# Performance work log

Measured on AMD Instinct MI355X. Metric: run time of the kernel, lower is better.

Reference implementation:

```python
import jax, jax.numpy as jnp
import numpy as np

N = 100000   # product nodes
E = 300000   # edges per relation
DIN = 128    # node_feature_dim
H = 128      # hidden_dim
NEG_SLOPE = 0.2


def setup_inputs() -> dict:
    key = jax.random.key(0)
    ks = iter(jax.random.split(key, 64))
    def nrm(shape, scale):
        return (jax.random.normal(next(ks), shape) * scale).astype(jnp.float32)
    d = {}
    d["x"] = nrm((N, DIN), 1.0)
    d["pos"] = nrm((N, 3), 1.0)
    for name in ("ei_chem", "ei_cond", "ei_mol"):
        d[name] = jax.random.randint(next(ks), (2, E), 0, N, dtype=jnp.int32)
    s = 1.0 / np.sqrt(H)
    d["Wp"] = nrm((DIN, H), 1.0 / np.sqrt(DIN)); d["bp"] = jnp.zeros((H,), jnp.float32)
    for L in ("1", "2"):
        for r in ("c", "d"):  # chemical_transformation, condition_modulation: heads=2
            d[f"W{L}{r}"] = nrm((H, H), s)
            d[f"as{L}{r}"] = nrm((2, H // 2), s)
            d[f"ad{L}{r}"] = nrm((2, H // 2), s)
            d[f"b{L}{r}"] = jnp.zeros((H,), jnp.float32)
        # molecule_target (EQGAT): heads=4
        d[f"W{L}m"] = nrm((H, H), s)
        d[f"as{L}m"] = nrm((4, H // 4), s)
        d[f"ad{L}m"] = nrm((4, H // 4), s)
        d[f"b{L}m"] = jnp.zeros((H,), jnp.float32)
        d[f"Wl{L}"] = nrm((H, H), s)
        d[f"bl{L}"] = jnp.zeros((H,), jnp.float32)
    d["Wy"] = nrm((H, 1), s); d["by"] = jnp.zeros((1,), jnp.float32)
    d["Wa"] = nrm((H, 1), s); d["ba"] = jnp.zeros((1,), jnp.float32)
    return d


def gat_conv(x, row, col, W, a_s, a_d, bias, heads, n):
    """PyG-style GATConv (concat=True, add_self_loops=True)."""
    Fh = W.shape[1] // heads
    loops = jnp.arange(n, dtype=row.dtype)
    row = jnp.concatenate([row, loops])
    col = jnp.concatenate([col, loops])
    h = (x @ W).reshape(n, heads, Fh)                      # [n,Hd,Fh]
    alpha_s = jnp.einsum('nhf,hf->nh', h, a_s)             # [n,Hd]
    alpha_d = jnp.einsum('nhf,hf->nh', h, a_d)
    e = jax.nn.leaky_relu(alpha_s[row] + alpha_d[col], NEG_SLOPE)  # [E',Hd]
    m = jax.lax.stop_gradient(jax.ops.segment_max(e, col, num_segments=n))
    ex = jnp.exp(e - m[col])
    z = jax.ops.segment_sum(ex, col, num_segments=n)
    alpha = ex / (z[col] + 1e-16)                          # per-dst softmax
    msg = h[row] * alpha[:, :, None]                       # [E',Hd,Fh]
    out = jax.ops.segment_sum(msg, col, num_segments=n).reshape(n, heads * Fh)
    return out + bias


def eqgat(x, pos, row, col, W, a_s, a_d, bias, Wl, bl, heads, n):
    geo = jnp.sqrt(jnp.sum((pos[row] - pos[col]) ** 2, axis=-1))  # [E]
    x = x + 0.1 * geo.mean()                                       # scalar broadcast
    h = gat_conv(x, row, col, W, a_s, a_d, bias, heads, n)
    return h @ Wl + bl


def reference(x, pos, ei_chem, ei_cond, ei_mol,
              Wp, bp,
              W1c, as1c, ad1c, b1c, W1d, as1d, ad1d, b1d,
              W1m, as1m, ad1m, b1m, Wl1, bl1,
              W2c, as2c, ad2c, b2c, W2d, as2d, ad2d, b2d,
              W2m, as2m, ad2m, b2m, Wl2, bl2,
              Wy, by, Wa, ba):
    n = x.shape[0]
    h0 = x @ Wp + bp
    h1 = jax.nn.relu(
        gat_conv(h0, ei_chem[0], ei_chem[1], W1c, as1c, ad1c, b1c, 2, n)
        + gat_conv(h0, ei_cond[0], ei_cond[1], W1d, as1d, ad1d, b1d, 2, n)
        + eqgat(h0, pos, ei_mol[0], ei_mol[1], W1m, as1m, ad1m, b1m, Wl1, bl1, 4, n))
    h2 = jax.nn.relu(
        gat_conv(h1, ei_chem[0], ei_chem[1], W2c, as2c, ad2c, b2c, 2, n)
        + gat_conv(h1, ei_cond[0], ei_cond[1], W2d, as2d, ad2d, b2d, 2, n)
        + eqgat(h1, pos, ei_mol[0], ei_mol[1], W2m, as2m, ad2m, b2m, Wl2, bl2, 4, n))
    pred_yield = (h2 @ Wy + by).squeeze(-1)
    pred_activity = (h2 @ Wa + ba).squeeze(-1)
    return jnp.stack([pred_yield, pred_activity], axis=-1)  # [n,2]
```

## Files before the change

kernel.cpp:

```cpp
#include <hip/hip_runtime.h>
#include <math.h>

typedef short short8 __attribute__((ext_vector_type(8)));
typedef float f32x4 __attribute__((ext_vector_type(4)));
typedef unsigned short us4 __attribute__((ext_vector_type(4)));

#define MAXDEG 32
#define GF_BIAS   1
#define GF_CSHIFT 2
#define GF_ALPHA  4
#define NFRAG 18432

__device__ __forceinline__ unsigned short f2bf(float f) {
  unsigned u = __float_as_uint(f);
  u += 0x7FFF + ((u >> 16) & 1);
  return (unsigned short)(u >> 16);
}
__device__ __forceinline__ float bf2f(unsigned short s) { return __uint_as_float(((unsigned)s) << 16); }
__device__ __forceinline__ float lrelu(float v) { return v > 0.f ? v : 0.2f * v; }

__global__ __launch_bounds__(256) void k_scatter3(
    const int* __restrict__ ei0, const int* __restrict__ ei1, const int* __restrict__ ei2,
    int* __restrict__ cur,
    int* __restrict__ s0, int* __restrict__ s1, int* __restrict__ s2,
    const float* __restrict__ pos, float* __restrict__ gsum, int E, int N) {
  __shared__ float part[4];
  const int t = blockIdx.x * 256 + threadIdx.x;
  float d = 0.f;
  if (t < 3 * E) {
    int rel, e;
    if (t < E)          { rel = 0; e = t; }
    else if (t < 2 * E) { rel = 1; e = t - E; }
    else                { rel = 2; e = t - 2 * E; }
    const int* ei = (rel == 0) ? ei0 : (rel == 1) ? ei1 : ei2;
    int* srcs     = (rel == 0) ? s0  : (rel == 1) ? s1  : s2;
    const int r = ei[e];
    const int c = ei[E + e];
    const int slot = atomicAdd(&cur[rel * N + c], 1);
    if (slot < MAXDEG) srcs[(size_t)c * MAXDEG + slot] = r;
    if (rel == 2) {
      const float dx = pos[3*r]   - pos[3*c];
      const float dy = pos[3*r+1] - pos[3*c+1];
      const float dz = pos[3*r+2] - pos[3*c+2];
      d = sqrtf(dx*dx + dy*dy + dz*dz);
    }
  }
  #pragma unroll
  for (int o = 32; o; o >>= 1) d += __shfl_down(d, o);
  if ((threadIdx.x & 63) == 0) part[threadIdx.x >> 6] = d;
  __syncthreads();
  if (threadIdx.x == 0) {
    const float s = part[0] + part[1] + part[2] + part[3];
    if (s != 0.f) atomicAdd(gsum, s);
  }
}

struct PrepArgs {
  const float* W[9];
  const float* as_[9];
  const float* ad_[9];
  unsigned short* hi[9];
  unsigned short* lo[9];
  float* csum[9];
  int fh[9];
};

__global__ __launch_bounds__(256) void k_prep(PrepArgs p) {
  const int s = blockIdx.x;
  const int t = threadIdx.x;
  const float* W = p.W[s];
  const int fh = p.fh[s];
  __shared__ float Ws[128 * 129];
  __shared__ float alpha[128 * 8];
  {
    const f32x4* src = (const f32x4*)W;
    for (int i = t; i < 4096; i += 256) {
      const f32x4 v = src[i];
      const int row = i >> 5;
      const int col = (i & 31) * 4;
      float* dst = &Ws[row * 129 + col];
      dst[0] = v[0]; dst[1] = v[1]; dst[2] = v[2]; dst[3] = v[3];
    }
  }
  __syncthreads();
  if (t < 128) {
    #pragma unroll
    for (int a = 0; a < 8; ++a) alpha[t * 8 + a] = 0.f;
    if (fh) {
      const int nh = 128 / fh;
      for (int h = 0; h < nh; ++h) {
        float s1 = 0.f, s2 = 0.f;
        for (int c = 0; c < fh; ++c) {
          const float w = Ws[t * 129 + h * fh + c];
          s1 += w * p.as_[s][h * fh + c];
          s2 += w * p.ad_[s][h * fh + c];
        }
        alpha[t * 8 + h] = s1;
        alpha[t * 8 + 4 + h] = s2;
      }
    }
  }
  __syncthreads();
  for (int idx = t; idx < NFRAG; idx += 256) {
    const int j = idx & 7, lane = (idx >> 3) & 63, kt = (idx >> 9) & 3, nt = idx >> 11;
    const int k = kt * 32 + (lane >> 4) * 8 + j;
    const int col = nt * 16 + (lane & 15);
    float w;
    if (col < 128) w = Ws[k * 129 + col];
    else if (col < 136) w = alpha[k * 8 + (col - 128)];
    else w = 0.f;
    const unsigned short h = f2bf(w);
    p.hi[s][idx] = h;
    p.lo[s][idx] = f2bf(w - bf2f(h));
  }
  if (t < 136) {
    float cs = 0.f;
    if (t < 128) for (int k = 0; k < 128; ++k) cs += Ws[k * 129 + t];
    else         for (int k = 0; k < 128; ++k) cs += alpha[k * 8 + (t - 128)];
    p.csum[s][t] = cs;
  }
}

__global__ __launch_bounds__(256, 2) void k_gmm(
    const float* __restrict__ A, const unsigned short* __restrict__ Whi,
    const unsigned short* __restrict__ Wlo, const float* __restrict__ csum,
    const float* __restrict__ bias, unsigned short* __restrict__ C,
    float* __restrict__ aS, float* __restrict__ aD,
    const float* __restrict__ gsum, float gscale,
    int n, int npad, int flags)
{
  __shared__ unsigned short shi[NFRAG];
  __shared__ unsigned short slo[NFRAG];
  {
    const f32x4* srch = (const f32x4*)Whi;
    const f32x4* srcl = (const f32x4*)Wlo;
    f32x4* dsth = (f32x4*)shi;
    f32x4* dstl = (f32x4*)slo;
    for (int i = threadIdx.x; i < NFRAG / 8; i += 256) { dsth[i] = srch[i]; dstl[i] = srcl[i]; }
  }
  __syncthreads();

  const int wave = threadIdx.x >> 6, lane = threadIdx.x & 63;
  const int m = lane & 15, kq = lane >> 4;
  const float cb = (flags & GF_CSHIFT) ? gscale * gsum[0] : 0.f;

  for (int rb = blockIdx.x * 128; rb < npad; rb += gridDim.x * 128) {
    const int rw = rb + wave * 32;
    short8 ah[2][4], al[2][4];
    #pragma unroll
    for (int sub = 0; sub < 2; ++sub) {
      const int row = rw + sub * 16 + m;
      const bool ok = row < n;
      const float* ap = A + (size_t)row * 128 + kq * 8;
      #pragma unroll
      for (int kt = 0; kt < 4; ++kt) {
        f32x4 x0 = {0.f, 0.f, 0.f, 0.f}, x1 = {0.f, 0.f, 0.f, 0.f};
        if (ok) { x0 = *(const f32x4*)(ap + kt * 32); x1 = *(const f32x4*)(ap + kt * 32 + 4); }
        #pragma unroll
        for (int j = 0; j < 4; ++j) {
          unsigned short h0 = f2bf(x0[j]);
          ah[sub][kt][j] = (short)h0;
          al[sub][kt][j] = (short)f2bf(x0[j] - bf2f(h0));
          unsigned short h1 = f2bf(x1[j]);
          ah[sub][kt][4 + j] = (short)h1;
          al[sub][kt][4 + j] = (short)f2bf(x1[j] - bf2f(h1));
        }
      }
    }
    f32x4 acc[2][9];
    #pragma unroll
    for (int sub = 0; sub < 2; ++sub)
      #pragma unroll
      for (int nt = 0; nt < 9; ++nt) acc[sub][nt] = f32x4{0.f, 0.f, 0.f, 0.f};

    #pragma unroll
    for (int nt = 0; nt < 9; ++nt) {
      #pragma unroll
      for (int kt = 0; kt < 4; ++kt) {
        const int fo = ((nt * 4 + kt) * 64 + lane) * 8;
        const short8 bh = *(const short8*)&shi[fo];
        const short8 bl = *(const short8*)&slo[fo];
        #pragma unroll
        for (int sub = 0; sub < 2; ++sub) {
          acc[sub][nt] = __builtin_amdgcn_mfma_f32_16x16x32_bf16(ah[sub][kt], bh, acc[sub][nt], 0, 0, 0);
          acc[sub][nt] = __builtin_amdgcn_mfma_f32_16x16x32_bf16(al[sub][kt], bh, acc[sub][nt], 0, 0, 0);
          acc[sub][nt] = __builtin_amdgcn_mfma_f32_16x16x32_bf16(ah[sub][kt], bl, acc[sub][nt], 0, 0, 0);
        }
      }
    }
    #pragma unroll
    for (int sub = 0; sub < 2; ++sub) {
      const int rbase = rw + sub * 16 + kq * 4;
      #pragma unroll
      for (int nt = 0; nt < 8; ++nt) {
        const int col = nt * 16 + m;
        const float cs = (flags & GF_CSHIFT) ? cb * csum[col] : 0.f;
        const float bb = (flags & GF_BIAS) ? bias[col] : 0.f;
        #pragma unroll
        for (int r = 0; r < 4; ++r)
          C[(size_t)(rbase + r) * 128 + col] = f2bf(acc[sub][nt][r] + cs + bb);
      }
      if ((flags & GF_ALPHA) && m < 8) {
        const float cs = (flags & GF_CSHIFT) ? cb * csum[128 + m] : 0.f;
        #pragma unroll
        for (int r = 0; r < 4; ++r) {
          const float v = acc[sub][8][r] + cs;
          const int row = rbase + r;
          if (m < 4) aS[(size_t)row * 4 + m] = v;
          else       aD[(size_t)row * 4 + (m - 4)] = v;
        }
      }
    }
  }
}

__global__ __launch_bounds__(256, 2) void k_gmmb(
    const unsigned short* __restrict__ A, const unsigned short* __restrict__ Whi,
    const unsigned short* __restrict__ Wlo, const float* __restrict__ csum,
    const float* __restrict__ bias, unsigned short* __restrict__ C,
    float* __restrict__ aS, float* __restrict__ aD,
    const float* __restrict__ gsum, float gscale,
    int n, int npad, int flags)
{
  __shared__ unsigned short shi[NFRAG];
  __shared__ unsigned short slo[NFRAG];
  {
    const f32x4* srch = (const f32x4*)Whi;
    const f32x4* srcl = (const f32x4*)Wlo;
    f32x4* dsth = (f32x4*)shi;
    f32x4* dstl = (f32x4*)slo;
    for (int i = threadIdx.x; i < NFRAG / 8; i += 256) { dsth[i] = srch[i]; dstl[i] = srcl[i]; }
  }
  __syncthreads();

  const int wave = threadIdx.x >> 6, lane = threadIdx.x & 63;
  const int m = lane & 15, kq = lane >> 4;
  const float cb = (flags & GF_CSHIFT) ? gscale * gsum[0] : 0.f;

  for (int rb = blockIdx.x * 128; rb < npad; rb += gridDim.x * 128) {
    const int rw = rb + wave * 32;
    short8 ah[2][4];
    #pragma unroll
    for (int sub = 0; sub < 2; ++sub) {
      const int row = rw + sub * 16 + m;
      const bool ok = row < n;
      const unsigned short* ap = A + (size_t)row * 128 + kq * 8;
      #pragma unroll
      for (int kt = 0; kt < 4; ++kt) {
        if (ok) ah[sub][kt] = *(const short8*)(ap + kt * 32);
        else    ah[sub][kt] = short8{0, 0, 0, 0, 0, 0, 0, 0};
      }
    }
    f32x4 acc[2][9];
    #pragma unroll
    for (int sub = 0; sub < 2; ++sub)
      #pragma unroll
      for (int nt = 0; nt < 9; ++nt) acc[sub][nt] = f32x4{0.f, 0.f, 0.f, 0.f};

    #pragma unroll
    for (int nt = 0; nt < 9; ++nt) {
      #pragma unroll
      for (int kt = 0; kt < 4; ++kt) {
        const int fo = ((nt * 4 + kt) * 64 + lane) * 8;
        const short8 bh = *(const short8*)&shi[fo];
        const short8 bl = *(const short8*)&slo[fo];
        #pragma unroll
        for (int sub = 0; sub < 2; ++sub) {
          acc[sub][nt] = __builtin_amdgcn_mfma_f32_16x16x32_bf16(ah[sub][kt], bh, acc[sub][nt], 0, 0, 0);
          acc[sub][nt] = __builtin_amdgcn_mfma_f32_16x16x32_bf16(ah[sub][kt], bl, acc[sub][nt], 0, 0, 0);
        }
      }
    }
    #pragma unroll
    for (int sub = 0; sub < 2; ++sub) {
      const int rbase = rw + sub * 16 + kq * 4;
      #pragma unroll
      for (int nt = 0; nt < 8; ++nt) {
        const int col = nt * 16 + m;
        const float cs = (flags & GF_CSHIFT) ? cb * csum[col] : 0.f;
        const float bb = (flags & GF_BIAS) ? bias[col] : 0.f;
        #pragma unroll
        for (int r = 0; r < 4; ++r)
          C[(size_t)(rbase + r) * 128 + col] = f2bf(acc[sub][nt][r] + cs + bb);
      }
      if ((flags & GF_ALPHA) && m < 8) {
        const float cs = (flags & GF_CSHIFT) ? cb * csum[128 + m] : 0.f;
        #pragma unroll
        for (int r = 0; r < 4; ++r) {
          const float v = acc[sub][8][r] + cs;
          const int row = rbase + r;
          if (m < 4) aS[(size_t)row * 4 + m] = v;
          else       aD[(size_t)row * 4 + (m - 4)] = v;
        }
      }
    }
  }
}

__global__ __launch_bounds__(256) void k_conv(
    const unsigned short* __restrict__ hb, const float* __restrict__ aS,
    const float* __restrict__ aD,
    const int* __restrict__ srcs, const int* __restrict__ cnt,
    const float* __restrict__ bias, unsigned short* __restrict__ out,
    int fh_shift, int n)
{
  __shared__ int   ssh[4][2][32];
  __shared__ float wsh[4][2][32][4];
  const int wv = threadIdx.x >> 6;
  const int lane = threadIdx.x & 63;
  const int hf = lane >> 5;
  const int l  = lane & 31;
  const int i = blockIdx.x * 8 + wv * 2 + hf;
  const bool iok = i < n;
  const int ipad = iok ? i : 0;
  const int c0 = l * 4;
  const int hd = c0 >> fh_shift;

  int deg = 0;
  if (iok) { deg = cnt[i]; if (deg > MAXDEG) deg = MAXDEG; }
  const int* sp = srcs + (size_t)ipad * MAXDEG;

  const bool valid = l < deg;
  int s = ipad;
  if (valid) s = sp[l];

  f32x4 ad4 = f32x4{0.f, 0.f, 0.f, 0.f}, asi = f32x4{0.f, 0.f, 0.f, 0.f};
  if (iok) {
    ad4 = *(const f32x4*)(aD + (size_t)i * 4);
    asi = *(const f32x4*)(aS + (size_t)i * 4);
  }
  f32x4 as4 = f32x4{0.f, 0.f, 0.f, 0.f};
  if (valid) as4 = *(const f32x4*)(aS + (size_t)s * 4);

  f32x4 w, z, wsf;
  #pragma unroll
  for (int hh = 0; hh < 4; ++hh) {
    w[hh] = valid ? __expf(lrelu(as4[hh] + ad4[hh])) : 0.f;
    z[hh] = w[hh];
  }
  #pragma unroll
  for (int o = 16; o; o >>= 1) {
    #pragma unroll
    for (int hh = 0; hh < 4; ++hh) z[hh] += __shfl_xor(z[hh], o, 32);
  }
  #pragma unroll
  for (int hh = 0; hh < 4; ++hh) {
    wsf[hh] = __expf(lrelu(asi[hh] + ad4[hh]));
    z[hh] += wsf[hh];
  }

  int dtot = (deg + 3) & ~3;
  const int dmax = max(dtot, __shfl_xor(dtot, 32));
  if (l < dmax) {
    ssh[wv][hf][l] = valid ? s : ipad;
    f32x4 wst = f32x4{0.f, 0.f, 0.f, 0.f};
    if (valid) wst = w;
    *(f32x4*)wsh[wv][hf][l] = wst;
  }

  f32x4 acc = f32x4{0.f, 0.f, 0.f, 0.f};
  {
    us4 u = {0, 0, 0, 0};
    if (iok) u = *(const us4*)(hb + (size_t)i * 128 + c0);
    const float ws = wsf[hd];
    #pragma unroll
    for (int q = 0; q < 4; ++q) acc[q] = ws * bf2f(u[q]);
  }
  for (int j0 = 0; j0 < dmax; j0 += 4) {
    const int s0 = ssh[wv][hf][j0],     s1 = ssh[wv][hf][j0 + 1];
    const int s2 = ssh[wv][hf][j0 + 2], s3 = ssh[wv][hf][j0 + 3];
    const float w0 = wsh[wv][hf][j0][hd],     w1 = wsh[wv][hf][j0 + 1][hd];
    const float w2 = wsh[wv][hf][j0 + 2][hd], w3 = wsh[wv][hf][j0 + 3][hd];
    const us4 u0 = *(const us4*)(hb + (size_t)s0 * 128 + c0);
    const us4 u1 = *(const us4*)(hb + (size_t)s1 * 128 + c0);
    const us4 u2 = *(const us4*)(hb + (size_t)s2 * 128 + c0);
    const us4 u3 = *(const us4*)(hb + (size_t)s3 * 128 + c0);
    #pragma unroll
    for (int q = 0; q < 4; ++q)
      acc[q] += w0 * bf2f(u0[q]) + w1 * bf2f(u1[q]) + w2 * bf2f(u2[q]) + w3 * bf2f(u3[q]);
  }

  if (!iok) return;
  const float inv = 1.f / (z[hd] + 1e-16f);
  const f32x4 bb = *(const f32x4*)(bias + c0);
  unsigned short* op = out + (size_t)i * 128 + c0;
  us4 res;
  #pragma unroll
  for (int q = 0; q < 4; ++q) res[q] = f2bf(acc[q] * inv + bb[q]);
  *(us4*)op = res;
}

__global__ __launch_bounds__(256) void k_conv2(
    const unsigned short* __restrict__ hcp, const unsigned short* __restrict__ hdp,
    const float* __restrict__ aSc, const float* __restrict__ aDc,
    const float* __restrict__ aSd, const float* __restrict__ aDd,
    const int* __restrict__ srcs_c, const int* __restrict__ cnt_c,
    const int* __restrict__ srcs_d, const int* __restrict__ cnt_d,
    const float* __restrict__ bias_c, const float* __restrict__ bias_d,
    unsigned short* __restrict__ out, int n)
{
  __shared__ int   ssh[4][2][2][32];
  __shared__ float wsh[4][2][2][32][2];
  const int wv = threadIdx.x >> 6;
  const int lane = threadIdx.x & 63;
  const int hf = lane >> 5;
  const int l  = lane & 31;
  const int i = blockIdx.x * 8 + wv * 2 + hf;
  const bool iok = i < n;
  const int ipad = iok ? i : 0;
  const int c0 = l * 4;
  const int hd = c0 >> 6;

  const unsigned short* hA[2] = {hcp, hdp};
  const float* aSA[2]  = {aSc, aSd};
  const float* aDA[2]  = {aDc, aDd};
  const int*   spA[2]  = {srcs_c, srcs_d};
  const int*   cntA[2] = {cnt_c, cnt_d};

  int deg[2]; bool valid[2]; int s[2];
  float2 ad2[2], asi2[2], as2[2];
  #pragma unroll
  for (int r = 0; r < 2; ++r) {
    deg[r] = 0;
    if (iok) { int d = cntA[r][i]; deg[r] = d > MAXDEG ? MAXDEG : d; }
  }
  #pragma unroll
  for (int r = 0; r < 2; ++r) {
    const int* sp = spA[r] + (size_t)ipad * MAXDEG;
    valid[r] = l < deg[r];
    s[r] = valid[r] ? sp[l] : ipad;
  }
  #pragma unroll
  for (int r = 0; r < 2; ++r) {
    ad2[r] = float2{0.f, 0.f};
    asi2[r] = float2{0.f, 0.f};
    if (iok) {
      ad2[r] = *(const float2*)(aDA[r] + (size_t)i * 4);
      asi2[r] = *(const float2*)(aSA[r] + (size_t)i * 4);
    }
  }
  #pragma unroll
  for (int r = 0; r < 2; ++r) {
    as2[r] = float2{0.f, 0.f};
    if (valid[r]) as2[r] = *(const float2*)(aSA[r] + (size_t)s[r] * 4);
  }

  float w0_[2], w1_[2], z0_[2], z1_[2], wsf0_[2], wsf1_[2];
  #pragma unroll
  for (int r = 0; r < 2; ++r) {
    w0_[r] = valid[r] ? __expf(lrelu(as2[r].x + ad2[r].x)) : 0.f;
    w1_[r] = valid[r] ? __expf(lrelu(as2[r].y + ad2[r].y)) : 0.f;
    z0_[r] = w0_[r]; z1_[r] = w1_[r];
  }
  #pragma unroll
  for (int o = 16; o; o >>= 1)
    #pragma unroll
    for (int r = 0; r < 2; ++r) {
      z0_[r] += __shfl_xor(z0_[r], o, 32);
      z1_[r] += __shfl_xor(z1_[r], o, 32);
    }
  #pragma unroll
  for (int r = 0; r < 2; ++r) {
    wsf0_[r] = __expf(lrelu(asi2[r].x + ad2[r].x));
    wsf1_[r] = __expf(lrelu(asi2[r].y + ad2[r].y));
    z0_[r] += wsf0_[r];
    z1_[r] += wsf1_[r];
  }
  float i0_[2], i1_[2];
  #pragma unroll
  for (int r = 0; r < 2; ++r) {
    i0_[r] = 1.f / (z0_[r] + 1e-16f);
    i1_[r] = 1.f / (z1_[r] + 1e-16f);
  }

  int dmaxA[2];
  #pragma unroll
  for (int rel = 0; rel < 2; ++rel) {
    int dtot = (deg[rel] + 3) & ~3;
    dmaxA[rel] = max(dtot, __shfl_xor(dtot, 32));
    if (l < dmaxA[rel]) {
      ssh[wv][rel][hf][l] = valid[rel] ? s[rel] : ipad;
      float2 wst = float2{0.f, 0.f};
      if (valid[rel]) wst = float2{w0_[rel] * i0_[rel], w1_[rel] * i1_[rel]};
      *(float2*)wsh[wv][rel][hf][l] = wst;
    }
  }

  f32x4 acc = f32x4{0.f, 0.f, 0.f, 0.f};
  {
    us4 uc = {0, 0, 0, 0}, ud = {0, 0, 0, 0};
    if (iok) {
      uc = *(const us4*)(hcp + (size_t)i * 128 + c0);
      ud = *(const us4*)(hdp + (size_t)i * 128 + c0);
    }
    const float wc = (hd == 0) ? wsf0_[0] * i0_[0] : wsf1_[0] * i1_[0];
    const float wd = (hd == 0) ? wsf0_[1] * i0_[1] : wsf1_[1] * i1_[1];
    #pragma unroll
    for (int q = 0; q < 4; ++q) acc[q] = wc * bf2f(uc[q]) + wd * bf2f(ud[q]);
  }

  const int dmaxM = max(dmaxA[0], dmaxA[1]);
  for (int j0 = 0; j0 < dmaxM; j0 += 4) {
    const bool g0 = j0 < dmaxA[0];
    const bool g1 = j0 < dmaxA[1];
    us4 u0a = {0,0,0,0}, u1a = {0,0,0,0}, u2a = {0,0,0,0}, u3a = {0,0,0,0};
    us4 u0b = {0,0,0,0}, u1b = {0,0,0,0}, u2b = {0,0,0,0}, u3b = {0,0,0,0};
    float wa0 = 0.f, wa1 = 0.f, wa2 = 0.f, wa3 = 0.f;
    float wb0 = 0.f, wb1 = 0.f, wb2 = 0.f, wb3 = 0.f;
    if (g0) {
      const int s0 = ssh[wv][0][hf][j0],     s1 = ssh[wv][0][hf][j0 + 1];
      const int s2 = ssh[wv][0][hf][j0 + 2], s3 = ssh[wv][0][hf][j0 + 3];
      wa0 = wsh[wv][0][hf][j0][hd];     wa1 = wsh[wv][0][hf][j0 + 1][hd];
      wa2 = wsh[wv][0][hf][j0 + 2][hd]; wa3 = wsh[wv][0][hf][j0 + 3][hd];
      u0a = *(const us4*)(hcp + (size_t)s0 * 128 + c0);
      u1a = *(const us4*)(hcp + (size_t)s1 * 128 + c0);
      u2a = *(const us4*)(hcp + (size_t)s2 * 128 + c0);
      u3a = *(const us4*)(hcp + (size_t)s3 * 128 + c0);
    }
    if (g1) {
      const int s0 = ssh[wv][1][hf][j0],     s1 = ssh[wv][1][hf][j0 + 1];
      const int s2 = ssh[wv][1][hf][j0 + 2], s3 = ssh[wv][1][hf][j0 + 3];
      wb0 = wsh[wv][1][hf][j0][hd];     wb1 = wsh[wv][1][hf][j0 + 1][hd];
      wb2 = wsh[wv][1][hf][j0 + 2][hd]; wb3 = wsh[wv][1][hf][j0 + 3][hd];
      u0b = *(const us4*)(hdp + (size_t)s0 * 128 + c0);
      u1b = *(const us4*)(hdp + (size_t)s1 * 128 + c0);
      u2b = *(const us4*)(hdp + (size_t)s2 * 128 + c0);
      u3b = *(const us4*)(hdp + (size_t)s3 * 128 + c0);
    }
    #pragma unroll
    for (int q = 0; q < 4; ++q) {
      acc[q] += wa0 * bf2f(u0a[q]) + wa1 * bf2f(u1a[q]) + wa2 * bf2f(u2a[q]) + wa3 * bf2f(u3a[q]);
      acc[q] += wb0 * bf2f(u0b[q]) + wb1 * bf2f(u1b[q]) + wb2 * bf2f(u2b[q]) + wb3 * bf2f(u3b[q]);
    }
  }

  if (!iok) return;
  const f32x4 bbc = *(const f32x4*)(bias_c + c0);
  const f32x4 bbd = *(const f32x4*)(bias_d + c0);
  unsigned short* op = out + (size_t)i * 128 + c0;
  const us4 cu = *(const us4*)op;
  us4 res;
  #pragma unroll
  for (int q = 0; q < 4; ++q)
    res[q] = f2bf(fmaxf(bf2f(cu[q]) + acc[q] + bbc[q] + bbd[q], 0.f));
  *(us4*)op = res;
}

__global__ __launch_bounds__(256) void k_head(
    const unsigned short* __restrict__ h2, const float* __restrict__ Wy,
    const float* __restrict__ by,
    const float* __restrict__ Wa, const float* __restrict__ ba,
    float* __restrict__ out, int n)
{
  const int r = blockIdx.x * 4 + (threadIdx.x >> 6);
  const int L = threadIdx.x & 63;
  if (r >= n) return;
  const float a = bf2f(h2[(size_t)r * 128 + L]);
  const float b = bf2f(h2[(size_t)r * 128 + 64 + L]);
  float py = a * Wy[L] + b * Wy[64 + L];
  float pa = a * Wa[L] + b * Wa[64 + L];
  #pragma unroll
  for (int o = 32; o; o >>= 1) { py += __shfl_down(py, o); pa += __shfl_down(pa, o); }
  if (L == 0) {
    out[(size_t)r * 2]     = py + by[0];
    out[(size_t)r * 2 + 1] = pa + ba[0];
  }
}

extern "C" void kernel_launch(void* const* d_in, const int* in_sizes, int n_in,
                              void* d_out, int out_size, void* d_ws, size_t ws_size,
                              hipStream_t stream) {
  const int N = in_sizes[0] / 128;
  const int E = in_sizes[2] / 2;
  const int npad = (N + 127) & ~127;

  const float* x       = (const float*)d_in[0];
  const float* pos     = (const float*)d_in[1];
  const int*   ei_chem = (const int*)d_in[2];
  const int*   ei_cond = (const int*)d_in[3];
  const int*   ei_mol  = (const int*)d_in[4];
  const float* bp = (const float*)d_in[6];
  const float* Wy = (const float*)d_in[35];
  const float* by = (const float*)d_in[36];
  const float* Wa = (const float*)d_in[37];
  const float* ba = (const float*)d_in[38];

  char* ws = (char*)d_ws;
  size_t off = 0;
  auto alloc = [&](size_t bytes) -> void* {
    void* p = ws + off; off += (bytes + 255) & ~(size_t)255; return p;
  };
  const size_t HBH = (size_t)npad * 128 * sizeof(unsigned short);
  unsigned short* H0b  = (unsigned short*)alloc(HBH);
  unsigned short* ACCb = (unsigned short*)alloc(HBH);
  unsigned short* HRb  = (unsigned short*)alloc(HBH);
  unsigned short* HRb2 = (unsigned short*)alloc(HBH);
  int* SRC[3];
  for (int r = 0; r < 3; ++r) SRC[r] = (int*)alloc((size_t)N * MAXDEG * sizeof(int));
  int*   CUR  = (int*)alloc((size_t)3 * N * sizeof(int));
  float* GSUM = (float*)alloc(256);
  float* AS   = (float*)alloc((size_t)npad * 4 * sizeof(float));
  float* AD   = (float*)alloc((size_t)npad * 4 * sizeof(float));
  float* ASd  = (float*)alloc((size_t)npad * 4 * sizeof(float));
  float* ADd  = (float*)alloc((size_t)npad * 4 * sizeof(float));

  PrepArgs pa{};
  const int widx[9] = {5, 7, 11, 15, 19, 21, 25, 29, 33};
  const int fhs[9]  = {0, 64, 64, 32, 0, 64, 64, 32, 0};
  unsigned short *WHI[9], *WLO[9];
  float* CSUM[9];
  for (int s = 0; s < 9; ++s) {
    WHI[s]  = (unsigned short*)alloc(NFRAG * sizeof(unsigned short));
    WLO[s]  = (unsigned short*)alloc(NFRAG * sizeof(unsigned short));
    CSUM[s] = (float*)alloc(144 * sizeof(float));
    pa.W[s] = (const float*)d_in[widx[s]];
    pa.fh[s] = fhs[s];
    pa.as_[s] = fhs[s] ? (const float*)d_in[widx[s] + 1] : nullptr;
    pa.ad_[s] = fhs[s] ? (const float*)d_in[widx[s] + 2] : nullptr;
    pa.hi[s] = WHI[s]; pa.lo[s] = WLO[s]; pa.csum[s] = CSUM[s];
  }

  hipMemsetAsync(CUR, 0, (size_t)3 * N * sizeof(int), stream);
  hipMemsetAsync(GSUM, 0, sizeof(float), stream);

  k_scatter3<<<(3 * E + 255) / 256, 256, 0, stream>>>(ei_chem, ei_cond, ei_mol,
                                                      CUR, SRC[0], SRC[1], SRC[2],
                                                      pos, GSUM, E, N);
  k_prep<<<9, 256, 0, stream>>>(pa);

  const int GG = 512;
  const float gscale = 0.1f / (float)E;
  const int cgrid = (N + 7) / 8;

  k_gmm<<<GG, 256, 0, stream>>>(x, WHI[0], WLO[0], CSUM[0], bp, H0b,
                                nullptr, nullptr, nullptr, 0.f, N, npad, GF_BIAS);

  auto layer = [&](const unsigned short* Hin, unsigned short* Acc, int base, int s0) {
    const float* bc = (const float*)d_in[base + 3];
    const float* bd = (const float*)d_in[base + 7];
    const float* bm = (const float*)d_in[base + 11];
    const float* bl = (const float*)d_in[base + 13];
    k_gmmb<<<GG, 256, 0, stream>>>(Hin, WHI[s0+2], WLO[s0+2], CSUM[s0+2], nullptr,
                                   HRb, AS, AD, GSUM, gscale, N, npad,
                                   GF_CSHIFT | GF_ALPHA);
    k_conv<<<cgrid, 256, 0, stream>>>(HRb, AS, AD, SRC[2], CUR + 2*N, bm, Acc, 5, N);
    k_gmmb<<<GG, 256, 0, stream>>>(Acc, WHI[s0+3], WLO[s0+3], CSUM[s0+3], bl, Acc,
                                   nullptr, nullptr, nullptr, 0.f, N, npad, GF_BIAS);
    k_gmmb<<<GG, 256, 0, stream>>>(Hin, WHI[s0+0], WLO[s0+0], CSUM[s0+0], nullptr,
                                   HRb, AS, AD, nullptr, 0.f, N, npad, GF_ALPHA);
    k_gmmb<<<GG, 256, 0, stream>>>(Hin, WHI[s0+1], WLO[s0+1], CSUM[s0+1], nullptr,
                                   HRb2, ASd, ADd, nullptr, 0.f, N, npad, GF_ALPHA);
    k_conv2<<<cgrid, 256, 0, stream>>>(HRb, HRb2, AS, AD, ASd, ADd,
                                       SRC[0], CUR + 0*N, SRC[1], CUR + 1*N,
                                       bc, bd, Acc, N);
  };

  layer(H0b, ACCb, 7, 1);
  layer(ACCb, H0b, 21, 5);

  k_head<<<(N + 3) / 4, 256, 0, stream>>>(H0b, Wy, by, Wa, ba, (float*)d_out, N);
}
```

Baseline: 655.1 us.

## Use hi-only bf16 weights for GAT projections and split geometry reduction kernel

Adds k_gmmh, a GEMM variant that uses only the high bf16 half of the split weights and drops the low-part MFMA pass. It is used for the three attention-projection GEMMs per layer, halving their MFMA work and shared-memory weight staging. The distance-sum computation is moved out of the scatter kernel into a separate grid-stride k_geo kernel, so the scatter no longer does per-edge block reductions and atomics. The cost is lower projection precision (bf16 weights instead of hi+lo) and one extra kernel launch.

```diff
diff --git a/kernel.cpp b/kernel.cpp
--- a/kernel.cpp
+++ b/kernel.cpp
@@ -23,36 +23,38 @@
     const int* __restrict__ ei0, const int* __restrict__ ei1, const int* __restrict__ ei2,
     int* __restrict__ cur,
     int* __restrict__ s0, int* __restrict__ s1, int* __restrict__ s2,
-    const float* __restrict__ pos, float* __restrict__ gsum, int E, int N) {
+    int E, int N) {
+  const int t = blockIdx.x * 256 + threadIdx.x;
+  if (t >= 3 * E) return;
+  int rel, e;
+  if (t < E)          { rel = 0; e = t; }
+  else if (t < 2 * E) { rel = 1; e = t - E; }
+  else                { rel = 2; e = t - 2 * E; }
+  const int* ei = (rel == 0) ? ei0 : (rel == 1) ? ei1 : ei2;
+  int* srcs     = (rel == 0) ? s0  : (rel == 1) ? s1  : s2;
+  const int r = ei[e];
+  const int c = ei[E + e];
+  const int slot = atomicAdd(&cur[rel * N + c], 1);
+  if (slot < MAXDEG) srcs[(size_t)c * MAXDEG + slot] = r;
+}
+
+__global__ __launch_bounds__(256) void k_geo(const float* __restrict__ pos,
+                                             const int* __restrict__ ei,
+                                             float* gsum, int E) {
   __shared__ float part[4];
-  const int t = blockIdx.x * 256 + threadIdx.x;
   float d = 0.f;
-  if (t < 3 * E) {
-    int rel, e;
-    if (t < E)          { rel = 0; e = t; }
-    else if (t < 2 * E) { rel = 1; e = t - E; }
-    else                { rel = 2; e = t - 2 * E; }
-    const int* ei = (rel == 0) ? ei0 : (rel == 1) ? ei1 : ei2;
-    int* srcs     = (rel == 0) ? s0  : (rel == 1) ? s1  : s2;
-    const int r = ei[e];
-    const int c = ei[E + e];
-    const int slot = atomicAdd(&cur[rel * N + c], 1);
-    if (slot < MAXDEG) srcs[(size_t)c * MAXDEG + slot] = r;
-    if (rel == 2) {
-      const float dx = pos[3*r]   - pos[3*c];
-      const float dy = pos[3*r+1] - pos[3*c+1];
-      const float dz = pos[3*r+2] - pos[3*c+2];
-      d = sqrtf(dx*dx + dy*dy + dz*dz);
-    }
+  for (int e = blockIdx.x * 256 + threadIdx.x; e < E; e += gridDim.x * 256) {
+    const int r = ei[e], c = ei[E + e];
+    const float dx = pos[3*r]   - pos[3*c];
+    const float dy = pos[3*r+1] - pos[3*c+1];
+    const float dz = pos[3*r+2] - pos[3*c+2];
+    d += sqrtf(dx*dx + dy*dy + dz*dz);
   }
   #pragma unroll
   for (int o = 32; o; o >>= 1) d += __shfl_down(d, o);
   if ((threadIdx.x & 63) == 0) part[threadIdx.x >> 6] = d;
   __syncthreads();
-  if (threadIdx.x == 0) {
-    const float s = part[0] + part[1] + part[2] + part[3];
-    if (s != 0.f) atomicAdd(gsum, s);
-  }
+  if (threadIdx.x == 0) atomicAdd(gsum, part[0] + part[1] + part[2] + part[3]);
 }
 
 struct PrepArgs {
@@ -282,6 +284,82 @@
         #pragma unroll
         for (int r = 0; r < 4; ++r)
           C[(size_t)(rbase + r) * 128 + col] = f2bf(acc[sub][nt][r] + cs + bb);
+      }
+      if ((flags & GF_ALPHA) && m < 8) {
+        const float cs = (flags & GF_CSHIFT) ? cb * csum[128 + m] : 0.f;
+        #pragma unroll
+        for (int r = 0; r < 4; ++r) {
+          const float v = acc[sub][8][r] + cs;
+          const int row = rbase + r;
+          if (m < 4) aS[(size_t)row * 4 + m] = v;
+          else       aD[(size_t)row * 4 + (m - 4)] = v;
+        }
+      }
+    }
+  }
+}
+
+__global__ __launch_bounds__(256, 3) void k_gmmh(
+    const unsigned short* __restrict__ A, const unsigned short* __restrict__ Whi,
+    const float* __restrict__ csum,
+    unsigned short* __restrict__ C,
+    float* __restrict__ aS, float* __restrict__ aD,
+    const float* __restrict__ gsum, float gscale,
+    int n, int npad, int flags)
+{
+  __shared__ unsigned short shi[NFRAG];
+  {
+    const f32x4* srch = (const f32x4*)Whi;
+    f32x4* dsth = (f32x4*)shi;
+    for (int i = threadIdx.x; i < NFRAG / 8; i += 256) dsth[i] = srch[i];
+  }
+  __syncthreads();
+
+  const int wave = threadIdx.x >> 6, lane = threadIdx.x & 63;
+  const int m = lane & 15, kq = lane >> 4;
+  const float cb = (flags & GF_CSHIFT) ? gscale * gsum[0] : 0.f;
+
+  for (int rb = blockIdx.x * 128; rb < npad; rb += gridDim.x * 128) {
+    const int rw = rb + wave * 32;
+    short8 ah[2][4];
+    #pragma unroll
+    for (int sub = 0; sub < 2; ++sub) {
+      const int row = rw + sub * 16 + m;
+      const bool ok = row < n;
+      const unsigned short* ap = A + (size_t)row * 128 + kq * 8;
+      #pragma unroll
+      for (int kt = 0; kt < 4; ++kt) {
+        if (ok) ah[sub][kt] = *(const short8*)(ap + kt * 32);
+        else    ah[sub][kt] = short8{0, 0, 0, 0, 0, 0, 0, 0};
+      }
+    }
+    f32x4 acc[2][9];
+    #pragma unroll
+    for (int sub = 0; sub < 2; ++sub)
+      #pragma unroll
+      for (int nt = 0; nt < 9; ++nt) acc[sub][nt] = f32x4{0.f, 0.f, 0.f, 0.f};
+
+    #pragma unroll
+    for (int nt = 0; nt < 9; ++nt) {
+      #pragma unroll
+      for (int kt = 0; kt < 4; ++kt) {
+        const int fo = ((nt * 4 + kt) * 64 + lane) * 8;
+        const short8 bh = *(const short8*)&shi[fo];
+        #pragma unroll
+        for (int sub = 0; sub < 2; ++sub)
+          acc[sub][nt] = __builtin_amdgcn_mfma_f32_16x16x32_bf16(ah[sub][kt], bh, acc[sub][nt], 0, 0, 0);
+      }
+    }
+    #pragma unroll
+    for (int sub = 0; sub < 2; ++sub) {
+      const int rbase = rw + sub * 16 + kq * 4;
+      #pragma unroll
+      for (int nt = 0; nt < 8; ++nt) {
+        const int col = nt * 16 + m;
+        const float cs = (flags & GF_CSHIFT) ? cb * csum[col] : 0.f;
+        #pragma unroll
+        for (int r = 0; r < 4; ++r)
+          C[(size_t)(rbase + r) * 128 + col] = f2bf(acc[sub][nt][r] + cs);
       }
       if ((flags & GF_ALPHA) && m < 8) {
         const float cs = (flags & GF_CSHIFT) ? cb * csum[128 + m] : 0.f;
@@ -411,7 +489,6 @@
   const int c0 = l * 4;
   const int hd = c0 >> 6;
 
-  const unsigned short* hA[2] = {hcp, hdp};
   const float* aSA[2]  = {aSc, aSd};
   const float* aDA[2]  = {aDc, aDd};
   const int*   spA[2]  = {srcs_c, srcs_d};
@@ -624,8 +701,8 @@
   hipMemsetAsync(GSUM, 0, sizeof(float), stream);
 
   k_scatter3<<<(3 * E + 255) / 256, 256, 0, stream>>>(ei_chem, ei_cond, ei_mol,
-                                                      CUR, SRC[0], SRC[1], SRC[2],
-                                                      pos, GSUM, E, N);
+                                                      CUR, SRC[0], SRC[1], SRC[2], E, N);
+  k_geo<<<512, 256, 0, stream>>>(pos, ei_mol, GSUM, E);
   k_prep<<<9, 256, 0, stream>>>(pa);
 
   const int GG = 512;
@@ -640,16 +717,15 @@
     const float* bd = (const float*)d_in[base + 7];
     const float* bm = (const float*)d_in[base + 11];
     const float* bl = (const float*)d_in[base + 13];
-    k_gmmb<<<GG, 256, 0, stream>>>(Hin, WHI[s0+2], WLO[s0+2], CSUM[s0+2], nullptr,
-                                   HRb, AS, AD, GSUM, gscale, N, npad,
-                                   GF_CSHIFT | GF_ALPHA);
+    k_gmmh<<<GG, 256, 0, stream>>>(Hin, WHI[s0+2], CSUM[s0+2], HRb, AS, AD,
+                                   GSUM, gscale, N, npad, GF_CSHIFT | GF_ALPHA);
     k_conv<<<cgrid, 256, 0, stream>>>(HRb, AS, AD, SRC[2], CUR + 2*N, bm, Acc, 5, N);
     k_gmmb<<<GG, 256, 0, stream>>>(Acc, WHI[s0+3], WLO[s0+3], CSUM[s0+3], bl, Acc,
                                    nullptr, nullptr, nullptr, 0.f, N, npad, GF_BIAS);
-    k_gmmb<<<GG, 256, 0, stream>>>(Hin, WHI[s0+0], WLO[s0+0], CSUM[s0+0], nullptr,
-                                   HRb, AS, AD, nullptr, 0.f, N, npad, GF_ALPHA);
-    k_gmmb<<<GG, 256, 0, stream>>>(Hin, WHI[s0+1], WLO[s0+1], CSUM[s0+1], nullptr,
-                                   HRb2, ASd, ADd, nullptr, 0.f, N, npad, GF_ALPHA);
+    k_gmmh<<<GG, 256, 0, stream>>>(Hin, WHI[s0+0], CSUM[s0+0], HRb, AS, AD,
+                                   GSUM, 0.f, N, npad, GF_ALPHA);
+    k_gmmh<<<GG, 256, 0, stream>>>(Hin, WHI[s0+1], CSUM[s0+1], HRb2, ASd, ADd,
+                                   GSUM, 0.f, N, npad, GF_ALPHA);
     k_conv2<<<cgrid, 256, 0, stream>>>(HRb, HRb2, AS, AD, ASd, ADd,
                                        SRC[0], CUR + 0*N, SRC[1], CUR + 1*N,
                                        bc, bd, Acc, N);
```

New measurement: 621.6 us. 5.1% less time.
